# Optimization experiments

Hardware: AMD Instinct MI355X
Metric: run time of the kernel (lower is better)

Reference implementation:

```python
import jax, jax.numpy as jnp
import numpy as np

B, S, D = 8, 2048, 1024
NEG_INF = jnp.float32(-1e30)  # stand-in for -inf; rows with all-masked are overwritten anyway


def setup_inputs() -> dict:
    key = jax.random.key(0)
    ks = jax.random.split(key, 10)
    query = jax.random.normal(ks[0], (B, S, D), dtype=jnp.float32)
    key_t = jax.random.normal(ks[1], (B, S, D), dtype=jnp.float32)
    value = jax.random.normal(ks[2], (B, S, D), dtype=jnp.float32)
    # pad mask: prefix of valid tokens per batch element (realistic ragged batch)
    lengths = jax.random.randint(ks[3], (B,), S // 2, S + 1)
    pad_masks = jnp.arange(S)[None, :] < lengths[:, None]  # (B, S) bool
    # causal mask, same lower-triangular pattern per batch element
    causal = jnp.tril(jnp.ones((S, S), dtype=bool))
    causal_masks = jnp.broadcast_to(causal, (B, S, S))
    # Linear params (torch nn.Linear: y = x @ W.T + b)
    scale = 0.02
    Wq = jax.random.normal(ks[4], (D, D), dtype=jnp.float32) * scale
    bq = jnp.zeros((D,), dtype=jnp.float32)
    Wk = jax.random.normal(ks[5], (D, D), dtype=jnp.float32) * scale
    bk = jnp.zeros((D,), dtype=jnp.float32)
    Wv = jax.random.normal(ks[6], (D, D), dtype=jnp.float32) * scale
    bv = jnp.zeros((D,), dtype=jnp.float32)
    return {"query": query, "key": key_t, "value": value,
            "pad_masks": pad_masks, "causal_masks": causal_masks,
            "Wq": Wq, "bq": bq, "Wk": Wk, "bk": bk, "Wv": Wv, "bv": bv}


def reference(query, key, value, pad_masks, causal_masks, Wq, bq, Wk, bk, Wv, bv):
    d_model = query.shape[-1]
    Q = jnp.einsum('bsd,ed->bse', query, Wq) + bq
    K = jnp.einsum('bsd,ed->bse', key, Wk) + bk
    V = jnp.einsum('bsd,ed->bse', value, Wv) + bv
    scores = jnp.einsum('bqd,bkd->bqk', Q, K) / jnp.sqrt(jnp.float32(d_model))
    combined = pad_masks[:, None, :] & causal_masks              # (B, S, S)
    row_any = jnp.any(combined, axis=-1, keepdims=True)          # (B, S, 1)
    scores = jnp.where(combined, scores, NEG_INF)
    scores = jnp.where(row_any, scores, jnp.zeros_like(scores))
    attn = jax.nn.softmax(scores, axis=-1)
    attn = jnp.where(row_any, attn, jnp.zeros_like(attn))
    # multiply by pad mask along the QUERY axis (faithful to the torch transpose)
    attn = attn * pad_masks[:, :, None].astype(attn.dtype)
    seq_emds = jnp.einsum('bqk,bkd->bqd', attn, V)
    return seq_emds, attn
```

## Files before the change

kernel.cpp:

```cpp
#include <hip/hip_runtime.h>
#include <hip/hip_bf16.h>

#define B_ 8
#define S_ 2048
#define D_ 1024
#define SCALE 0.03125f

typedef __attribute__((ext_vector_type(4))) float f32x4;
typedef __attribute__((ext_vector_type(8))) short short8;
typedef __attribute__((ext_vector_type(4))) short short4v;

static __device__ inline unsigned short f2bf(float f) {
    unsigned int u = __float_as_uint(f);
    u += 0x7FFF + ((u >> 16) & 1);
    return (unsigned short)(u >> 16);
}

static __device__ __forceinline__ void gload16(const void* g, void* l) {
    __builtin_amdgcn_global_load_lds(
        (const __attribute__((address_space(1))) unsigned int*)g,
        (__attribute__((address_space(3))) unsigned int*)l, 16, 0, 0);
}

__global__ void lengths_kernel(const unsigned char* __restrict__ pm, int* __restrict__ lens) {
    __shared__ int cnt[B_];
    int tid = threadIdx.x;
    if (tid < B_) cnt[tid] = 0;
    __syncthreads();
    int layout;
    if (pm[0] == 1 && pm[1] == 1) layout = 0;
    else if (pm[0] == 1) layout = 1;
    else layout = 2;
    for (int i = tid; i < B_ * S_; i += blockDim.x) {
        bool v;
        if (layout == 0) v = pm[i] != 0;
        else if (layout == 1) v = ((const int*)pm)[i] != 0;
        else v = ((const float*)pm)[i] != 0.0f;
        if (v) atomicAdd(&cnt[i >> 11], 1);
    }
    __syncthreads();
    if (tid < B_) lens[tid] = cnt[tid];
}

__global__ void convert_kernel(const float* __restrict__ X, unsigned short* __restrict__ Xb,
                               const float* __restrict__ W, unsigned short* __restrict__ Wb) {
    const int z = blockIdx.z;
    const float* src = z ? W : X;
    unsigned short* dst = z ? Wb : Xb;
    const int n = z ? (D_ * D_) : (B_ * S_ * D_);
    int idx = (blockIdx.x * 256 + threadIdx.x) * 8;
    if (idx >= n) return;
    float4 a = *(const float4*)(src + idx);
    float4 b = *(const float4*)(src + idx + 4);
    short8 o;
    o[0] = (short)f2bf(a.x); o[1] = (short)f2bf(a.y);
    o[2] = (short)f2bf(a.z); o[3] = (short)f2bf(a.w);
    o[4] = (short)f2bf(b.x); o[5] = (short)f2bf(b.y);
    o[6] = (short)f2bf(b.z); o[7] = (short)f2bf(b.w);
    *(short8*)(dst + idx) = o;
}

__global__ void proj_bf16_kernel(const unsigned short* __restrict__ Xb,
                                 const unsigned short* __restrict__ Wb,
                                 const float* __restrict__ bias,
                                 unsigned short* __restrict__ O,
                                 unsigned short* __restrict__ Vt,
                                 int trans) {
    __shared__ unsigned short As[128 * 32];
    __shared__ unsigned short Bs[128 * 32];

    const int m0 = blockIdx.y * 128;
    const int n0 = blockIdx.x * 128;
    const int tid = threadIdx.x;
    const int lane = tid & 63, w = tid >> 6;
    const int wr = w >> 1, wc = w & 1;
    const int g = lane >> 4, l15 = lane & 15;

    f32x4 acc[4][4];
    const f32x4 z4 = {0.f, 0.f, 0.f, 0.f};
    for (int a = 0; a < 4; ++a)
        for (int b2 = 0; b2 < 4; ++b2) acc[a][b2] = z4;

    for (int kk = 0; kk < D_; kk += 32) {
#pragma unroll
        for (int t = 0; t < 2; ++t) {
            int flat = (w * 2 + t) * 1024 + lane * 16;
            int row = flat >> 6, colb = flat & 63;
            const char* ga = (const char*)Xb + ((size_t)(m0 + row) * D_ + kk) * 2 + colb;
            const char* gb = (const char*)Wb + ((size_t)(n0 + row) * D_ + kk) * 2 + colb;
            gload16(ga, (char*)As + (w * 2 + t) * 1024);
            gload16(gb, (char*)Bs + (w * 2 + t) * 1024);
        }
        asm volatile("s_waitcnt vmcnt(0)" ::: "memory");
        __syncthreads();
        short8 a_frag[4], b_frag[4];
#pragma unroll
        for (int mf = 0; mf < 4; ++mf)
            a_frag[mf] = *(const short8*)(&As[(wr * 64 + mf * 16 + l15) * 32 + g * 8]);
#pragma unroll
        for (int nf = 0; nf < 4; ++nf)
            b_frag[nf] = *(const short8*)(&Bs[(wc * 64 + nf * 16 + l15) * 32 + g * 8]);
#pragma unroll
        for (int mf = 0; mf < 4; ++mf)
#pragma unroll
            for (int nf = 0; nf < 4; ++nf)
                acc[mf][nf] = __builtin_amdgcn_mfma_f32_16x16x32_bf16(a_frag[mf], b_frag[nf], acc[mf][nf], 0, 0, 0);
        __syncthreads();
    }

    if (!trans) {
#pragma unroll
        for (int mf = 0; mf < 4; ++mf) {
#pragma unroll
            for (int nf = 0; nf < 4; ++nf) {
                int gm = m0 + wr * 64 + mf * 16 + 4 * g;
                int gn = n0 + wc * 64 + nf * 16 + l15;
                float bb = bias[gn];
#pragma unroll
                for (int i = 0; i < 4; ++i)
                    O[(size_t)(gm + i) * D_ + gn] = f2bf(acc[mf][nf][i] + bb);
            }
        }
    } else {
#pragma unroll
        for (int mf = 0; mf < 4; ++mf) {
#pragma unroll
            for (int nf = 0; nf < 4; ++nf) {
                int gm = m0 + wr * 64 + mf * 16 + 4 * g;
                int b = gm >> 11, tok = gm & 2047;
                int gn = n0 + wc * 64 + nf * 16 + l15;
                float bb = bias[gn];
                short4v sv;
#pragma unroll
                for (int i = 0; i < 4; ++i) sv[i] = (short)f2bf(acc[mf][nf][i] + bb);
                *(short4v*)(&Vt[((size_t)b * D_ + gn) * S_ + tok]) = sv;
            }
        }
    }
}

__global__ void proj_kernel(const float* __restrict__ q, const float* __restrict__ k,
                            const float* __restrict__ v,
                            const float* __restrict__ Wq, const float* __restrict__ Wk,
                            const float* __restrict__ Wv,
                            const float* __restrict__ bq, const float* __restrict__ bk,
                            const float* __restrict__ bv,
                            unsigned short* __restrict__ Qb, unsigned short* __restrict__ Kb,
                            unsigned short* __restrict__ Vt) {
    const int z = blockIdx.z;
    const float* X = (z == 0) ? q : (z == 1) ? k : v;
    const float* W = (z == 0) ? Wq : (z == 1) ? Wk : Wv;
    const float* bias = (z == 0) ? bq : (z == 1) ? bk : bv;

    __shared__ short As[128 * 40];
    __shared__ short Bs[128 * 40];

    const int m0 = blockIdx.y * 128;
    const int n0 = blockIdx.x * 128;
    const int tid = threadIdx.x;
    const int lane = tid & 63, wid = tid >> 6;
    const int wr = wid >> 1, wc = wid & 1;
    const int g = lane >> 4, l15 = lane & 15;

    f32x4 acc[4][4];
    const f32x4 z4 = {0.f, 0.f, 0.f, 0.f};
    for (int a = 0; a < 4; ++a)
        for (int b2 = 0; b2 < 4; ++b2) acc[a][b2] = z4;

    for (int kk = 0; kk < D_; kk += 32) {
#pragma unroll
        for (int it = 0; it < 4; ++it) {
            int flat = it * 1024 + tid * 4;
            int r = flat >> 5, c = flat & 31;
            float4 va = *(const float4*)(X + (size_t)(m0 + r) * D_ + kk + c);
            short4v sa = {(short)f2bf(va.x), (short)f2bf(va.y), (short)f2bf(va.z), (short)f2bf(va.w)};
            *(short4v*)(&As[r * 40 + c]) = sa;
            float4 vb = *(const float4*)(W + (size_t)(n0 + r) * D_ + kk + c);
            short4v sb = {(short)f2bf(vb.x), (short)f2bf(vb.y), (short)f2bf(vb.z), (short)f2bf(vb.w)};
            *(short4v*)(&Bs[r * 40 + c]) = sb;
        }
        __syncthreads();
        short8 a_frag[4], b_frag[4];
#pragma unroll
        for (int mf = 0; mf < 4; ++mf)
            a_frag[mf] = *(const short8*)(&As[(wr * 64 + mf * 16 + l15) * 40 + g * 8]);
#pragma unroll
        for (int nf = 0; nf < 4; ++nf)
            b_frag[nf] = *(const short8*)(&Bs[(wc * 64 + nf * 16 + l15) * 40 + g * 8]);
#pragma unroll
        for (int mf = 0; mf < 4; ++mf)
#pragma unroll
            for (int nf = 0; nf < 4; ++nf)
                acc[mf][nf] = __builtin_amdgcn_mfma_f32_16x16x32_bf16(a_frag[mf], b_frag[nf], acc[mf][nf], 0, 0, 0);
        __syncthreads();
    }

    if (z < 2) {
        unsigned short* O = (z == 0) ? Qb : Kb;
#pragma unroll
        for (int mf = 0; mf < 4; ++mf) {
#pragma unroll
            for (int nf = 0; nf < 4; ++nf) {
                int gm = m0 + wr * 64 + mf * 16 + 4 * g;
                int gn = n0 + wc * 64 + nf * 16 + l15;
                float bb = bias[gn];
#pragma unroll
                for (int i = 0; i < 4; ++i)
                    O[(size_t)(gm + i) * D_ + gn] = f2bf(acc[mf][nf][i] + bb);
            }
        }
    } else {
#pragma unroll
        for (int mf = 0; mf < 4; ++mf) {
#pragma unroll
            for (int nf = 0; nf < 4; ++nf) {
                int gm = m0 + wr * 64 + mf * 16 + 4 * g;
                int b = gm >> 11, tok = gm & 2047;
                int gn = n0 + wc * 64 + nf * 16 + l15;
                float bb = bias[gn];
                short4v sv;
#pragma unroll
                for (int i = 0; i < 4; ++i) sv[i] = (short)f2bf(acc[mf][nf][i] + bb);
                *(short4v*)(&Vt[((size_t)b * D_ + gn) * S_ + tok]) = sv;
            }
        }
    }
}

__global__ void scores_kernel(const unsigned short* __restrict__ Qb,
                              const unsigned short* __restrict__ Kb,
                              const int* __restrict__ lens,
                              float* __restrict__ attn) {
    const int b = blockIdx.y;
    const int idx = blockIdx.x;
    int qt = (int)((sqrtf(8.f * idx + 1.f) - 1.f) * 0.5f);
    while ((qt + 1) * (qt + 2) / 2 <= idx) ++qt;
    while (qt * (qt + 1) / 2 > idx) --qt;
    const int kt = idx - qt * (qt + 1) / 2;
    const int m0 = qt * 128, n0 = kt * 128;
    const int len = lens[b];
    if (m0 >= len) return;

    __shared__ unsigned short As[128 * 32];
    __shared__ unsigned short Bs[128 * 32];

    const int tid = threadIdx.x;
    const int lane = tid & 63, w = tid >> 6;
    const int wr = w >> 1, wc = w & 1;
    const int g = lane >> 4, l15 = lane & 15;

    const char* Qbase = (const char*)(Qb + (size_t)(b * S_ + m0) * D_);
    const char* Kbase = (const char*)(Kb + (size_t)(b * S_ + n0) * D_);

    f32x4 acc[4][4];
    const f32x4 z4 = {0.f, 0.f, 0.f, 0.f};
    for (int a = 0; a < 4; ++a)
        for (int b2 = 0; b2 < 4; ++b2) acc[a][b2] = z4;

    for (int kk = 0; kk < D_; kk += 32) {
#pragma unroll
        for (int t = 0; t < 2; ++t) {
            int flat = (w * 2 + t) * 1024 + lane * 16;
            int row = flat >> 6, colb = flat & 63;
            gload16(Qbase + (size_t)row * (D_ * 2) + kk * 2 + colb, (char*)As + (w * 2 + t) * 1024);
            gload16(Kbase + (size_t)row * (D_ * 2) + kk * 2 + colb, (char*)Bs + (w * 2 + t) * 1024);
        }
        asm volatile("s_waitcnt vmcnt(0)" ::: "memory");
        __syncthreads();
        short8 a_frag[4], b_frag[4];
#pragma unroll
        for (int mf = 0; mf < 4; ++mf)
            a_frag[mf] = *(const short8*)(&As[(wr * 64 + mf * 16 + l15) * 32 + g * 8]);
#pragma unroll
        for (int nf = 0; nf < 4; ++nf)
            b_frag[nf] = *(const short8*)(&Bs[(wc * 64 + nf * 16 + l15) * 32 + g * 8]);
#pragma unroll
        for (int mf = 0; mf < 4; ++mf)
#pragma unroll
            for (int nf = 0; nf < 4; ++nf)
                acc[mf][nf] = __builtin_amdgcn_mfma_f32_16x16x32_bf16(a_frag[mf], b_frag[nf], acc[mf][nf], 0, 0, 0);
        __syncthreads();
    }

#pragma unroll
    for (int mf = 0; mf < 4; ++mf) {
#pragma unroll
        for (int nf = 0; nf < 4; ++nf) {
            int gm = m0 + wr * 64 + mf * 16 + 4 * g;
            int gn = n0 + wc * 64 + nf * 16 + l15;
#pragma unroll
            for (int i = 0; i < 4; ++i) {
                int rq = gm + i;
                if (rq < len && gn <= rq)
                    attn[(size_t)(b * S_ + rq) * S_ + gn] = acc[mf][nf][i] * SCALE;
            }
        }
    }
}

__global__ void softmax_kernel(const int* __restrict__ lens,
                               float* __restrict__ attn, unsigned short* __restrict__ P) {
    const int row = blockIdx.x;
    const int b = row >> 11, qpos = row & 2047;
    const int tid = threadIdx.x;
    const size_t rbase = (size_t)row * S_;
    if (qpos >= lens[b]) {
        short8 z = {0, 0, 0, 0, 0, 0, 0, 0};
        *(short8*)(&P[rbase + (size_t)tid * 8]) = z;
        return;
    }
    __shared__ float wm[4], wl[4];
    const int c0 = tid * 8;
    float4 a0 = *(const float4*)(attn + rbase + c0);
    float4 a1 = *(const float4*)(attn + rbase + c0 + 4);
    float x[8] = {a0.x, a0.y, a0.z, a0.w, a1.x, a1.y, a1.z, a1.w};
    float lmax = -1e30f;
#pragma unroll
    for (int j = 0; j < 8; ++j) {
        if (c0 + j > qpos) x[j] = -1e30f;
        lmax = fmaxf(lmax, x[j]);
    }
#pragma unroll
    for (int off = 1; off < 64; off <<= 1) lmax = fmaxf(lmax, __shfl_xor(lmax, off));
    if ((tid & 63) == 0) wm[tid >> 6] = lmax;
    __syncthreads();
    const float m = fmaxf(fmaxf(wm[0], wm[1]), fmaxf(wm[2], wm[3]));
    float e[8];
    float lsum = 0.f;
#pragma unroll
    for (int j = 0; j < 8; ++j) {
        e[j] = (x[j] > -1e29f) ? __expf(x[j] - m) : 0.f;
        lsum += e[j];
    }
#pragma unroll
    for (int off = 1; off < 64; off <<= 1) lsum += __shfl_xor(lsum, off);
    if ((tid & 63) == 0) wl[tid >> 6] = lsum;
    __syncthreads();
    const float inv = 1.0f / (wl[0] + wl[1] + wl[2] + wl[3]);
    float4 o0, o1;
    short8 pb;
#pragma unroll
    for (int j = 0; j < 8; ++j) {
        float p = e[j] * inv;
        ((float*)&o0)[j < 4 ? j : 0] = 0.f;
        pb[j] = (short)f2bf(p);
        e[j] = p;
    }
    o0.x = e[0]; o0.y = e[1]; o0.z = e[2]; o0.w = e[3];
    o1.x = e[4]; o1.y = e[5]; o1.z = e[6]; o1.w = e[7];
    *(float4*)(attn + rbase + c0) = o0;
    *(float4*)(attn + rbase + c0 + 4) = o1;
    *(short8*)(&P[rbase + c0]) = pb;
}

__global__ void pv_kernel(const unsigned short* __restrict__ P,
                          const unsigned short* __restrict__ Vt,
                          const int* __restrict__ lens, float* __restrict__ seq) {
    const int b = blockIdx.z;
    const int q0 = blockIdx.y * 128;
    const int n0 = blockIdx.x * 128;
    const int len = lens[b];
    const int tid = threadIdx.x;

    if (q0 >= len) {
        const float4 zf = {0.f, 0.f, 0.f, 0.f};
#pragma unroll
        for (int it = 0; it < 16; ++it) {
            int flat = it * 1024 + tid * 4;
            int r = flat >> 7, c = flat & 127;
            *(float4*)(&seq[(size_t)(b * S_ + q0 + r) * D_ + n0 + c]) = zf;
        }
        return;
    }

    __shared__ unsigned short As[128 * 32];
    __shared__ unsigned short Bs[128 * 32];
    const int lane = tid & 63, w = tid >> 6;
    const int wr = w >> 1, wc = w & 1;
    const int g = lane >> 4, l15 = lane & 15;

    f32x4 acc[4][4];
    const f32x4 z4 = {0.f, 0.f, 0.f, 0.f};
    for (int a = 0; a < 4; ++a)
        for (int b2 = 0; b2 < 4; ++b2) acc[a][b2] = z4;

    const char* Pbase = (const char*)(P + (size_t)(b * S_ + q0) * S_);
    const char* Vbase = (const char*)(Vt + ((size_t)b * D_ + n0) * S_);

    const int nkt = (q0 + 128) / 32;
    for (int kt = 0; kt < nkt; ++kt) {
        int k0 = kt * 32;
#pragma unroll
        for (int t = 0; t < 2; ++t) {
            int flat = (w * 2 + t) * 1024 + lane * 16;
            int row = flat >> 6, colb = flat & 63;
            gload16(Pbase + (size_t)row * (S_ * 2) + k0 * 2 + colb, (char*)As + (w * 2 + t) * 1024);
            gload16(Vbase + (size_t)row * (S_ * 2) + k0 * 2 + colb, (char*)Bs + (w * 2 + t) * 1024);
        }
        asm volatile("s_waitcnt vmcnt(0)" ::: "memory");
        __syncthreads();
        short8 a_frag[4], b_frag[4];
#pragma unroll
        for (int mf = 0; mf < 4; ++mf)
            a_frag[mf] = *(const short8*)(&As[(wr * 64 + mf * 16 + l15) * 32 + g * 8]);
#pragma unroll
        for (int nf = 0; nf < 4; ++nf)
            b_frag[nf] = *(const short8*)(&Bs[(wc * 64 + nf * 16 + l15) * 32 + g * 8]);
#pragma unroll
        for (int mf = 0; mf < 4; ++mf)
#pragma unroll
            for (int nf = 0; nf < 4; ++nf)
                acc[mf][nf] = __builtin_amdgcn_mfma_f32_16x16x32_bf16(a_frag[mf], b_frag[nf], acc[mf][nf], 0, 0, 0);
        __syncthreads();
    }

#pragma unroll
    for (int mf = 0; mf < 4; ++mf) {
#pragma unroll
        for (int nf = 0; nf < 4; ++nf) {
            int gq = q0 + wr * 64 + mf * 16 + 4 * g;
            int gn = n0 + wc * 64 + nf * 16 + l15;
#pragma unroll
            for (int i = 0; i < 4; ++i)
                seq[(size_t)(b * S_ + gq + i) * D_ + gn] = acc[mf][nf][i];
        }
    }
}

extern "C" void kernel_launch(void* const* d_in, const int* in_sizes, int n_in,
                              void* d_out, int out_size, void* d_ws, size_t ws_size,
                              hipStream_t stream) {
    const float* q = (const float*)d_in[0];
    const float* k = (const float*)d_in[1];
    const float* v = (const float*)d_in[2];
    const unsigned char* pm = (const unsigned char*)d_in[3];
    const float* Wq = (const float*)d_in[5];
    const float* bq = (const float*)d_in[6];
    const float* Wk = (const float*)d_in[7];
    const float* bk = (const float*)d_in[8];
    const float* Wv = (const float*)d_in[9];
    const float* bv = (const float*)d_in[10];

    float* seq = (float*)d_out;
    float* attn = seq + (size_t)B_ * S_ * D_;

    char* ws = (char*)d_ws;
    int* lens = (int*)ws;
    unsigned short* Qb = (unsigned short*)(ws + 256);
    unsigned short* Kb = Qb + (size_t)B_ * S_ * D_;
    unsigned short* Vt = Kb + (size_t)B_ * S_ * D_;
    unsigned short* Xb = Vt + (size_t)B_ * D_ * S_;
    unsigned short* Wb = Xb + (size_t)B_ * S_ * D_;
    unsigned short* P = Qb;

    const size_t need = 256 + 5ull * B_ * S_ * D_ * 2 + (size_t)D_ * D_ * 2;

    hipMemsetAsync(attn, 0, (size_t)B_ * S_ * S_ * sizeof(float), stream);
    lengths_kernel<<<1, 256, 0, stream>>>(pm, lens);

    if (ws_size >= need) {
        const float* Xs[3] = {q, k, v};
        const float* Wsrc[3] = {Wq, Wk, Wv};
        const float* Bsrc[3] = {bq, bk, bv};
        for (int z = 0; z < 3; ++z) {
            convert_kernel<<<dim3(B_ * S_ * D_ / 2048, 1, 2), 256, 0, stream>>>(
                Xs[z], Xb, Wsrc[z], Wb);
            proj_bf16_kernel<<<dim3(D_ / 128, (B_ * S_) / 128), 256, 0, stream>>>(
                Xb, Wb, Bsrc[z],
                (z == 0) ? Qb : (z == 1) ? Kb : (unsigned short*)nullptr,
                (z == 2) ? Vt : (unsigned short*)nullptr,
                (z == 2) ? 1 : 0);
        }
    } else {
        proj_kernel<<<dim3(D_ / 128, (B_ * S_) / 128, 3), 256, 0, stream>>>(
            q, k, v, Wq, Wk, Wv, bq, bk, bv, Qb, Kb, Vt);
    }

    scores_kernel<<<dim3(136, B_), 256, 0, stream>>>(Qb, Kb, lens, attn);
    softmax_kernel<<<dim3(B_ * S_), 256, 0, stream>>>(lens, attn, P);
    pv_kernel<<<dim3(D_ / 128, S_ / 128, B_), 256, 0, stream>>>(P, Vt, lens, seq);
}
```

Measured before the change: 473.1 us.

## Drop attn memset and batch QKV conversion and projection into single launches

Removes the full-size zero fill of the attention output. Padded query rows are now zeroed inside the softmax kernel, and valid rows are already fully rewritten there. Merges the three convert launches and the three projection launches into one launch each, using blockIdx.z to pick Q, K or V. This removes a large memory write pass and per-launch serialization. The cost is a larger workspace for all three bf16 inputs, and if the workspace is too small the code falls back to the slow fp32 path.

```diff
diff --git a/kernel.cpp b/kernel.cpp
--- a/kernel.cpp
+++ b/kernel.cpp
@@ -42,12 +42,25 @@
     if (tid < B_) lens[tid] = cnt[tid];
 }
 
-__global__ void convert_kernel(const float* __restrict__ X, unsigned short* __restrict__ Xb,
-                               const float* __restrict__ W, unsigned short* __restrict__ Wb) {
+__global__ void convert_all_kernel(const float* __restrict__ q, const float* __restrict__ k,
+                                   const float* __restrict__ v,
+                                   const float* __restrict__ Wq, const float* __restrict__ Wk,
+                                   const float* __restrict__ Wv,
+                                   unsigned short* __restrict__ Xb,
+                                   unsigned short* __restrict__ Wb) {
     const int z = blockIdx.z;
-    const float* src = z ? W : X;
-    unsigned short* dst = z ? Wb : Xb;
-    const int n = z ? (D_ * D_) : (B_ * S_ * D_);
+    const float* src;
+    unsigned short* dst;
+    int n;
+    if (z < 3) {
+        src = (z == 0) ? q : (z == 1) ? k : v;
+        dst = Xb + (size_t)z * B_ * S_ * D_;
+        n = B_ * S_ * D_;
+    } else {
+        src = (z == 3) ? Wq : (z == 4) ? Wk : Wv;
+        dst = Wb + (size_t)(z - 3) * D_ * D_;
+        n = D_ * D_;
+    }
     int idx = (blockIdx.x * 256 + threadIdx.x) * 8;
     if (idx >= n) return;
     float4 a = *(const float4*)(src + idx);
@@ -60,12 +73,18 @@
     *(short8*)(dst + idx) = o;
 }
 
-__global__ void proj_bf16_kernel(const unsigned short* __restrict__ Xb,
-                                 const unsigned short* __restrict__ Wb,
-                                 const float* __restrict__ bias,
-                                 unsigned short* __restrict__ O,
-                                 unsigned short* __restrict__ Vt,
-                                 int trans) {
+__global__ void proj_bf16_kernel(const unsigned short* __restrict__ Xb3,
+                                 const unsigned short* __restrict__ Wb3,
+                                 const float* __restrict__ bq, const float* __restrict__ bk,
+                                 const float* __restrict__ bv,
+                                 unsigned short* __restrict__ Qb,
+                                 unsigned short* __restrict__ Kb,
+                                 unsigned short* __restrict__ Vt) {
+    const int z = blockIdx.z;
+    const unsigned short* Xb = Xb3 + (size_t)z * B_ * S_ * D_;
+    const unsigned short* Wb = Wb3 + (size_t)z * D_ * D_;
+    const float* bias = (z == 0) ? bq : (z == 1) ? bk : bv;
+
     __shared__ unsigned short As[128 * 32];
     __shared__ unsigned short Bs[128 * 32];
 
@@ -108,7 +127,8 @@
         __syncthreads();
     }
 
-    if (!trans) {
+    if (z < 2) {
+        unsigned short* O = (z == 0) ? Qb : Kb;
 #pragma unroll
         for (int mf = 0; mf < 4; ++mf) {
 #pragma unroll
@@ -304,13 +324,16 @@
     const int b = row >> 11, qpos = row & 2047;
     const int tid = threadIdx.x;
     const size_t rbase = (size_t)row * S_;
+    const int c0 = tid * 8;
     if (qpos >= lens[b]) {
         short8 z = {0, 0, 0, 0, 0, 0, 0, 0};
-        *(short8*)(&P[rbase + (size_t)tid * 8]) = z;
+        *(short8*)(&P[rbase + c0]) = z;
+        const float4 zf = {0.f, 0.f, 0.f, 0.f};
+        *(float4*)(attn + rbase + c0) = zf;
+        *(float4*)(attn + rbase + c0 + 4) = zf;
         return;
     }
     __shared__ float wm[4], wl[4];
-    const int c0 = tid * 8;
     float4 a0 = *(const float4*)(attn + rbase + c0);
     float4 a1 = *(const float4*)(attn + rbase + c0 + 4);
     float x[8] = {a0.x, a0.y, a0.z, a0.w, a1.x, a1.y, a1.z, a1.w};
@@ -341,10 +364,8 @@
     short8 pb;
 #pragma unroll
     for (int j = 0; j < 8; ++j) {
-        float p = e[j] * inv;
-        ((float*)&o0)[j < 4 ? j : 0] = 0.f;
-        pb[j] = (short)f2bf(p);
-        e[j] = p;
+        e[j] *= inv;
+        pb[j] = (short)f2bf(e[j]);
     }
     o0.x = e[0]; o0.y = e[1]; o0.z = e[2]; o0.w = e[3];
     o1.x = e[4]; o1.y = e[5]; o1.z = e[6]; o1.w = e[7];
@@ -450,27 +471,18 @@
     unsigned short* Kb = Qb + (size_t)B_ * S_ * D_;
     unsigned short* Vt = Kb + (size_t)B_ * S_ * D_;
     unsigned short* Xb = Vt + (size_t)B_ * D_ * S_;
-    unsigned short* Wb = Xb + (size_t)B_ * S_ * D_;
+    unsigned short* Wb = Xb + 3ull * B_ * S_ * D_;
     unsigned short* P = Qb;
 
-    const size_t need = 256 + 5ull * B_ * S_ * D_ * 2 + (size_t)D_ * D_ * 2;
-
-    hipMemsetAsync(attn, 0, (size_t)B_ * S_ * S_ * sizeof(float), stream);
+    const size_t need = 256 + 6ull * B_ * S_ * D_ * 2 + 3ull * D_ * D_ * 2;
+
     lengths_kernel<<<1, 256, 0, stream>>>(pm, lens);
 
     if (ws_size >= need) {
-        const float* Xs[3] = {q, k, v};
-        const float* Wsrc[3] = {Wq, Wk, Wv};
-        const float* Bsrc[3] = {bq, bk, bv};
-        for (int z = 0; z < 3; ++z) {
-            convert_kernel<<<dim3(B_ * S_ * D_ / 2048, 1, 2), 256, 0, stream>>>(
-                Xs[z], Xb, Wsrc[z], Wb);
-            proj_bf16_kernel<<<dim3(D_ / 128, (B_ * S_) / 128), 256, 0, stream>>>(
-                Xb, Wb, Bsrc[z],
-                (z == 0) ? Qb : (z == 1) ? Kb : (unsigned short*)nullptr,
-                (z == 2) ? Vt : (unsigned short*)nullptr,
-                (z == 2) ? 1 : 0);
-        }
+        convert_all_kernel<<<dim3(B_ * S_ * D_ / 2048, 1, 6), 256, 0, stream>>>(
+            q, k, v, Wq, Wk, Wv, Xb, Wb);
+        proj_bf16_kernel<<<dim3(D_ / 128, (B_ * S_) / 128, 3), 256, 0, stream>>>(
+            Xb, Wb, bq, bk, bv, Qb, Kb, Vt);
     } else {
         proj_kernel<<<dim3(D_ / 128, (B_ * S_) / 128, 3), 256, 0, stream>>>(
             q, k, v, Wq, Wk, Wv, bq, bk, bv, Qb, Kb, Vt);
```

Result: faster. 451.8 us (-4.5%).
